# Kernel tuning notes

Measured on AMD Instinct MI355X. Metric: run time of the kernel, lower is better.

Reference implementation:

```python
import math
import jax, jax.numpy as jnp
import numpy as np

B, N, D, Pd, L, H = 2, 384, 256, 64, 8, 8
Dh = D // H
VOCAB = 21


def _layernorm(x, w, b, eps=1e-5):
    m = jnp.mean(x, axis=-1, keepdims=True)
    v = jnp.var(x, axis=-1, keepdims=True)
    return (x - m) * jax.lax.rsqrt(v + eps) * w + b


def _safe_norm(v):
    return jnp.sqrt(jnp.sum(v * v, axis=-1, keepdims=True) + 1e-8)


def _rot6d(r6):
    # Zhou et al. 6D rotation -> 3x3 via Gram-Schmidt (rows b1,b2,b3)
    a1, a2 = r6[..., :3], r6[..., 3:6]
    b1 = a1 / _safe_norm(a1)
    a2p = a2 - jnp.sum(b1 * a2, axis=-1, keepdims=True) * b1
    b2 = a2p / _safe_norm(a2p)
    b3 = jnp.cross(b1, b2)
    return jnp.stack([b1, b2, b3], axis=-2)  # [..., 3, 3]


def _pos_enc(n, d):
    pos = jnp.arange(n, dtype=jnp.float32)[:, None]
    div = jnp.exp(jnp.arange(0, d, 2, dtype=jnp.float32) * (-math.log(10000.0) / d))
    ang = pos * div  # [n, d/2]
    return jnp.zeros((n, d), jnp.float32).at[:, 0::2].set(jnp.sin(ang)).at[:, 1::2].set(jnp.cos(ang))


def _se3_frame_attention(Q, K, V, frames):
    # Frame-conditioned attention: dot-product scores biased by squared
    # distance between frame translations (IPA-style point bias).
    t = frames[..., :3, 3]                                   # [B,N,3]
    d2 = jnp.sum((t[:, :, None] - t[:, None, :]) ** 2, -1)   # [B,N,N]
    s = jnp.einsum('bihd,bjhd->bhij', Q, K) / math.sqrt(Dh) - d2[:, None]
    a = jax.nn.softmax(s, axis=-1)
    return jnp.einsum('bhij,bjhd->bihd', a, V)               # [B,N,H,Dh]


def _encode(tokens, tok_emb, emb_ln_w, emb_ln_b, Wq, Wk, Wv, Wo, bo,
            attn_ln_w, attn_ln_b, ff_ln_w, ff_ln_b, W1, b1, W2, b2,
            Wop, bop, relpos_emb, pair_ln_w, pair_ln_b, Wf1, bf1, Wf2, bf2):
    Bb, Nn = tokens.shape
    x = tok_emb[tokens] + _pos_enc(Nn, D)[None]
    x = _layernorm(x, emb_ln_w, emb_ln_b)
    frames = jnp.broadcast_to(jnp.eye(4, dtype=x.dtype), (Bb, Nn, 4, 4))
    pos = jnp.arange(Nn)
    rel = jnp.clip(pos[None, :] - pos[:, None], -64, 64) + 64  # rel[i,j]=pos[j]-pos[i]
    rel_e = relpos_emb[rel]                                    # [N,N,Pd]
    bot = jnp.broadcast_to(jnp.array([0.0, 0.0, 0.0, 1.0], x.dtype), (Bb, Nn, 1, 4))
    for l in range(L):
        # SE3 attention block (dropout = identity in eval)
        Q = (x @ Wq[l]).reshape(Bb, Nn, H, Dh)
        Kh = (x @ Wk[l]).reshape(Bb, Nn, H, Dh)
        Vh = (x @ Wv[l]).reshape(Bb, Nn, H, Dh)
        ao = _se3_frame_attention(Q, Kh, Vh, frames).reshape(Bb, Nn, D)
        x = _layernorm(x + ao @ Wo[l] + bo[l], attn_ln_w[l], attn_ln_b[l])
        # FFN (pre-LN inside the Sequential), residual add
        h = _layernorm(x, ff_ln_w[l], ff_ln_b[l])
        x = x + (jax.nn.gelu(h @ W1[l] + b1[l], approximate=False) @ W2[l] + b2[l])
        # Pair features
        proj = jax.nn.relu(x @ Wop + bop)                      # [B,N,Pd]
        pair = _layernorm(proj[:, :, None] + proj[:, None, :] + rel_e[None],
                          pair_ln_w, pair_ln_b)                # [B,N,N,Pd]
        # Frame head
        feat = jnp.concatenate([x, pair.mean(axis=2)], axis=-1)
        raw = jax.nn.silu(feat @ Wf1 + bf1) @ Wf2 + bf2        # [B,N,9]
        R = _rot6d(raw[..., :6])
        trans = raw[..., 6:]
        top = jnp.concatenate([R, trans[..., None]], axis=-1)  # [B,N,3,4]
        frames = jnp.concatenate([top, bot], axis=-2)          # [B,N,4,4]
    return frames, x


def setup_inputs() -> dict:
    key = jax.random.key(0)
    ks = iter(jax.random.split(key, 16))
    def w(shape, scale):
        return (jax.random.normal(next(ks), shape) * scale).astype(jnp.float32)
    return {
        'tokens': jax.random.randint(next(ks), (B, N), 0, VOCAB, dtype=jnp.int32),
        'tok_emb': w((VOCAB, D), 0.02),
        'emb_ln_w': jnp.ones((D,), jnp.float32), 'emb_ln_b': jnp.zeros((D,), jnp.float32),
        'Wq': w((L, D, D), D ** -0.5), 'Wk': w((L, D, D), D ** -0.5),
        'Wv': w((L, D, D), D ** -0.5), 'Wo': w((L, D, D), D ** -0.5),
        'bo': jnp.zeros((L, D), jnp.float32),
        'attn_ln_w': jnp.ones((L, D), jnp.float32), 'attn_ln_b': jnp.zeros((L, D), jnp.float32),
        'ff_ln_w': jnp.ones((L, D), jnp.float32), 'ff_ln_b': jnp.zeros((L, D), jnp.float32),
        'W1': w((L, D, 4 * D), D ** -0.5), 'b1': jnp.zeros((L, 4 * D), jnp.float32),
        'W2': w((L, 4 * D, D), (4 * D) ** -0.5), 'b2': jnp.zeros((L, D), jnp.float32),
        'Wop': w((D, Pd), D ** -0.5), 'bop': jnp.zeros((Pd,), jnp.float32),
        'relpos_emb': w((129, Pd), 0.02),
        'pair_ln_w': jnp.ones((Pd,), jnp.float32), 'pair_ln_b': jnp.zeros((Pd,), jnp.float32),
        'Wf1': w((D + Pd, 128), (D + Pd) ** -0.5), 'bf1': jnp.zeros((128,), jnp.float32),
        'Wf2': w((128, 9), 128 ** -0.5), 'bf2': jnp.zeros((9,), jnp.float32),
    }


def reference(tokens, tok_emb, emb_ln_w, emb_ln_b, Wq, Wk, Wv, Wo, bo,
              attn_ln_w, attn_ln_b, ff_ln_w, ff_ln_b, W1, b1, W2, b2,
              Wop, bop, relpos_emb, pair_ln_w, pair_ln_b, Wf1, bf1, Wf2, bf2):
    return _encode(tokens, tok_emb, emb_ln_w, emb_ln_b, Wq, Wk, Wv, Wo, bo,
                   attn_ln_w, attn_ln_b, ff_ln_w, ff_ln_b, W1, b1, W2, b2,
                   Wop, bop, relpos_emb, pair_ln_w, pair_ln_b, Wf1, bf1, Wf2, bf2)
```

## Files before the change

### kernel.cpp

```cpp
#include <hip/hip_runtime.h>
#include <hip/hip_bf16.h>
#include <math.h>

#define B_  2
#define N_  384
#define D_  256
#define PD_ 64
#define L_  8
#define H_  8
#define DH_ 32
#define GR  4
#define IT  8
#define RT_ 132

__global__ void prologue_kernel(const int* __restrict__ tokens, const float* __restrict__ tok_emb,
                                const float* __restrict__ lnw, const float* __restrict__ lnb,
                                const float* __restrict__ relpos,
                                float* __restrict__ x, float* __restrict__ frames,
                                float* __restrict__ tx, float* __restrict__ ty,
                                float* __restrict__ tz,
                                float* __restrict__ relc, float* __restrict__ relcT) {
  int row = blockIdx.x;
  int n = row % N_;
  int d = threadIdx.x;
  __shared__ float rbuf[256];
  __shared__ float smr;
  if (d < 16) frames[row * 16 + d] = (d == 0 || d == 5 || d == 10 || d == 15) ? 1.0f : 0.0f;
  if (d == 16) tx[row] = 0.0f;
  if (d == 17) ty[row] = 0.0f;
  if (d == 18) tz[row] = 0.0f;
  if (row < 129 && d >= 192) {
    int lane = d & 63;
    float s = relpos[row * PD_ + lane];
    #pragma unroll
    for (int off = 32; off >= 1; off >>= 1) s += __shfl_xor(s, off, 64);
    if (lane == 0) smr = s * (1.0f / PD_);
  }
  int tok = tokens[row];
  float val = tok_emb[tok * D_ + d];
  int i = d >> 1;
  float dv = expf((float)(2 * i) * (-logf(10000.0f) / (float)D_));
  float ang = (float)n * dv;
  val += (d & 1) ? cosf(ang) : sinf(ang);
  rbuf[d] = val; __syncthreads();
  for (int s = 128; s > 0; s >>= 1) { if (d < s) rbuf[d] += rbuf[d + s]; __syncthreads(); }
  float mean = rbuf[0] / D_;
  __syncthreads();
  rbuf[d] = val * val; __syncthreads();
  for (int s = 128; s > 0; s >>= 1) { if (d < s) rbuf[d] += rbuf[d + s]; __syncthreads(); }
  float var = rbuf[0] / D_ - mean * mean;
  float r = rsqrtf(var + 1e-5f);
  x[row * D_ + d] = (val - mean) * r * lnw[d] + lnb[d];
  if (row < 129 && d < PD_) {
    float cv = relpos[row * PD_ + d] - smr;
    relc[row * PD_ + d] = cv;
    relcT[d * RT_ + row] = cv;
  }
}

__device__ __forceinline__ void qkv_unit(int bid, int tid, const float* __restrict__ x,
                                         const float* __restrict__ Wq, const float* __restrict__ Wk,
                                         const float* __restrict__ Wv,
                                         float* __restrict__ q, float* __restrict__ kt,
                                         float* __restrict__ v, float* sA) {
  int tile = bid & 3;
  int m = (bid >> 2) % 3;
  int r0 = (bid / 12) * GR;
  float* red = sA + GR * D_;
  {
    int r = tid >> 6, lane = tid & 63;
    ((float4*)(sA + r * D_))[lane] = ((const float4*)(x + (size_t)(r0 + r) * D_))[lane];
  }
  __syncthreads();
  const float* W = (m == 0) ? Wq : (m == 1) ? Wk : Wv;
  int kc = tid >> 6, c = tid & 63;
  const float* wp = W + (size_t)(kc * 64) * D_ + tile * 64 + c;
  const float* s0 = sA + kc * 64;
  float a0 = 0.f, a1 = 0.f, a2 = 0.f, a3 = 0.f;
  for (int kk = 0; kk < 64; kk += 4) {
    float w0 = wp[(size_t)kk * D_], w1 = wp[(size_t)(kk + 1) * D_];
    float w2 = wp[(size_t)(kk + 2) * D_], w3 = wp[(size_t)(kk + 3) * D_];
    float4 h0 = *(const float4*)(s0 + 0 * D_ + kk);
    float4 h1 = *(const float4*)(s0 + 1 * D_ + kk);
    float4 h2 = *(const float4*)(s0 + 2 * D_ + kk);
    float4 h3 = *(const float4*)(s0 + 3 * D_ + kk);
    a0 = fmaf(h0.x, w0, fmaf(h0.y, w1, fmaf(h0.z, w2, fmaf(h0.w, w3, a0))));
    a1 = fmaf(h1.x, w0, fmaf(h1.y, w1, fmaf(h1.z, w2, fmaf(h1.w, w3, a1))));
    a2 = fmaf(h2.x, w0, fmaf(h2.y, w1, fmaf(h2.z, w2, fmaf(h2.w, w3, a2))));
    a3 = fmaf(h3.x, w0, fmaf(h3.y, w1, fmaf(h3.z, w2, fmaf(h3.w, w3, a3))));
  }
  red[(kc * 4 + 0) * 64 + c] = a0;
  red[(kc * 4 + 1) * 64 + c] = a1;
  red[(kc * 4 + 2) * 64 + c] = a2;
  red[(kc * 4 + 3) * 64 + c] = a3;
  __syncthreads();
  int r = tid >> 6;
  float s = red[(0 * 4 + r) * 64 + c] + red[(1 * 4 + r) * 64 + c]
          + red[(2 * 4 + r) * 64 + c] + red[(3 * 4 + r) * 64 + c];
  int col = tile * 64 + c;
  int row = r0 + r;
  if (m == 1) {
    int b = row / N_, j = row % N_;
    int hh = col >> 5, dd = col & 31;
    kt[((size_t)(b * H_ + hh) * DH_ + dd) * N_ + j] = s;
  } else {
    float* O = (m == 0) ? q : v;
    O[(size_t)row * D_ + col] = s;
  }
}

__device__ __forceinline__ void proj_unit(int row, int tid, const float* __restrict__ x,
                                          const float* __restrict__ Wop, const float* __restrict__ bop,
                                          float* __restrict__ projc, float* __restrict__ projcT,
                                          float* smem) {
  float* sA  = smem;
  float* red = smem + 256;
  if (tid < 64) ((float4*)sA)[tid] = ((const float4*)(x + (size_t)row * D_))[tid];
  __syncthreads();
  int kc = tid >> 6, c = tid & 63;
  const float* wp = Wop + (kc * 64) * PD_ + c;
  const float* s0 = sA + kc * 64;
  float a0 = 0.f, a1 = 0.f, a2 = 0.f, a3 = 0.f;
  for (int kk = 0; kk < 64; kk += 4) {
    a0 = fmaf(s0[kk],     wp[(kk)     * PD_], a0);
    a1 = fmaf(s0[kk + 1], wp[(kk + 1) * PD_], a1);
    a2 = fmaf(s0[kk + 2], wp[(kk + 2) * PD_], a2);
    a3 = fmaf(s0[kk + 3], wp[(kk + 3) * PD_], a3);
  }
  red[kc * 64 + c] = (a0 + a1) + (a2 + a3);
  __syncthreads();
  if (tid < 64) {
    float acc = fmaxf(bop[tid] + red[tid] + red[64 + tid] + red[128 + tid] + red[192 + tid], 0.0f);
    float s = acc;
    #pragma unroll
    for (int off = 32; off >= 1; off >>= 1) s += __shfl_xor(s, off, 64);
    float cv = acc - s * (1.0f / PD_);
    projc[row * PD_ + tid] = cv;
    projcT[(size_t)tid * (B_ * N_) + row] = cv;
  }
}

__global__ void qkv_kernel(const float* __restrict__ x, const float* __restrict__ Wq,
                           const float* __restrict__ Wk, const float* __restrict__ Wv,
                           float* __restrict__ q, float* __restrict__ kt, float* __restrict__ v) {
  __shared__ __align__(16) float smem[2048];
  qkv_unit(blockIdx.x, threadIdx.x, x, Wq, Wk, Wv, q, kt, v, smem);
}

__global__ void proj_qkv_kernel(const float* __restrict__ x,
                                const float* __restrict__ Wop, const float* __restrict__ bop,
                                float* __restrict__ projc, float* __restrict__ projcT,
                                const float* __restrict__ Wq, const float* __restrict__ Wk,
                                const float* __restrict__ Wv,
                                float* __restrict__ q, float* __restrict__ kt,
                                float* __restrict__ v) {
  __shared__ __align__(16) float smem[2048];
  int bid = blockIdx.x, tid = threadIdx.x;
  if (bid < B_ * N_) proj_unit(bid, tid, x, Wop, bop, projc, projcT, smem);
  else               qkv_unit(bid - B_ * N_, tid, x, Wq, Wk, Wv, q, kt, v, smem);
}

__global__ void wo_ln_kernel(const float* __restrict__ ao, const float* __restrict__ Wo,
                             const float* __restrict__ bo,
                             const float* __restrict__ lnw, const float* __restrict__ lnb,
                             float* xio, float* __restrict__ xout) {
  int r0 = blockIdx.x * 2;
  int tid = threadIdx.x;
  int wave = tid >> 6, lane = tid & 63;
  __shared__ __align__(16) float sAO[2 * D_];
  __shared__ float wred[4][4];
  if (tid < 128) ((float4*)sAO)[tid] = ((const float4*)(ao + (size_t)r0 * D_))[tid];
  __syncthreads();
  const float* wp = Wo + tid;
  float a0 = 0.f, a1 = 0.f, a2 = 0.f, a3 = 0.f;
  float c0 = 0.f, c1 = 0.f, c2 = 0.f, c3 = 0.f;
  for (int kk = 0; kk < D_; kk += 4) {
    float w0 = wp[(size_t)kk * D_], w1 = wp[(size_t)(kk + 1) * D_];
    float w2 = wp[(size_t)(kk + 2) * D_], w3 = wp[(size_t)(kk + 3) * D_];
    float4 h0 = *(const float4*)(sAO + kk);
    float4 h1 = *(const float4*)(sAO + D_ + kk);
    a0 = fmaf(h0.x, w0, a0); a1 = fmaf(h0.y, w1, a1);
    a2 = fmaf(h0.z, w2, a2); a3 = fmaf(h0.w, w3, a3);
    c0 = fmaf(h1.x, w0, c0); c1 = fmaf(h1.y, w1, c1);
    c2 = fmaf(h1.z, w2, c2); c3 = fmaf(h1.w, w3, c3);
  }
  float bb = bo[tid];
  float v0 = xio[(size_t)r0 * D_ + tid]       + bb + (a0 + a1) + (a2 + a3);
  float v1 = xio[(size_t)(r0 + 1) * D_ + tid] + bb + (c0 + c1) + (c2 + c3);
  float s0 = v0, q0 = v0 * v0, s1 = v1, q1 = v1 * v1;
  #pragma unroll
  for (int off = 32; off >= 1; off >>= 1) {
    s0 += __shfl_xor(s0, off, 64); q0 += __shfl_xor(q0, off, 64);
    s1 += __shfl_xor(s1, off, 64); q1 += __shfl_xor(q1, off, 64);
  }
  if (lane == 0) {
    wred[0][wave] = s0; wred[1][wave] = q0;
    wred[2][wave] = s1; wred[3][wave] = q1;
  }
  __syncthreads();
  float S0 = wred[0][0] + wred[0][1] + wred[0][2] + wred[0][3];
  float Q0 = wred[1][0] + wred[1][1] + wred[1][2] + wred[1][3];
  float S1 = wred[2][0] + wred[2][1] + wred[2][2] + wred[2][3];
  float Q1 = wred[3][0] + wred[3][1] + wred[3][2] + wred[3][3];
  float m0 = S0 * (1.0f / D_), m1 = S1 * (1.0f / D_);
  float r0v = rsqrtf(Q0 * (1.0f / D_) - m0 * m0 + 1e-5f);
  float r1v = rsqrtf(Q1 * (1.0f / D_) - m1 * m1 + 1e-5f);
  float wv = lnw[tid], bv = lnb[tid];
  xout[(size_t)r0 * D_ + tid]       = (v0 - m0) * r0v * wv + bv;
  xout[(size_t)(r0 + 1) * D_ + tid] = (v1 - m1) * r1v * wv + bv;
  xio[(size_t)r0 * D_ + tid]       = 0.0f;
  xio[(size_t)(r0 + 1) * D_ + tid] = 0.0f;
}

__global__ void ff_fused_kernel(const float* __restrict__ xs,
                                const float* __restrict__ lnw, const float* __restrict__ lnb,
                                const float* __restrict__ W1, const float* __restrict__ b1,
                                const float* __restrict__ W2, const float* __restrict__ b2v,
                                float* __restrict__ xacc) {
  int bid = blockIdx.x;
  int tile = bid & 7;
  int r0 = (bid >> 3) * GR;
  int tid = threadIdx.x;
  __shared__ __align__(16) float sA[GR * D_];
  __shared__ float red[2 * GR * 128];
  __shared__ __align__(16) float sF[128 * 4];
  {
    int r = tid >> 6, lane = tid & 63;
    float4 v = ((const float4*)(xs + (size_t)(r0 + r) * D_))[lane];
    float s = v.x + v.y + v.z + v.w;
    float s2 = v.x * v.x + v.y * v.y + v.z * v.z + v.w * v.w;
    #pragma unroll
    for (int off = 32; off >= 1; off >>= 1) {
      s  += __shfl_xor(s, off, 64);
      s2 += __shfl_xor(s2, off, 64);
    }
    float mean = s * (1.0f / D_);
    float var = s2 * (1.0f / D_) - mean * mean;
    float rin = rsqrtf(var + 1e-5f);
    float4 w4 = ((const float4*)lnw)[lane];
    float4 b4 = ((const float4*)lnb)[lane];
    float4 nv;
    nv.x = (v.x - mean) * rin * w4.x + b4.x;
    nv.y = (v.y - mean) * rin * w4.y + b4.y;
    nv.z = (v.z - mean) * rin * w4.z + b4.z;
    nv.w = (v.w - mean) * rin * w4.w + b4.w;
    ((float4*)(sA + r * D_))[lane] = nv;
  }
  __syncthreads();
  {
    int kc = tid >> 7, c = tid & 127;
    int col = tile * 128 + c;
    const float* wp = W1 + (size_t)(kc * 128) * 1024 + col;
    const float* s0 = sA + kc * 128;
    float a0 = 0.f, a1 = 0.f, a2 = 0.f, a3 = 0.f;
    for (int kk = 0; kk < 128; kk += 4) {
      float w0 = wp[(size_t)kk * 1024], w1 = wp[(size_t)(kk + 1) * 1024];
      float w2 = wp[(size_t)(kk + 2) * 1024], w3 = wp[(size_t)(kk + 3) * 1024];
      float4 h0 = *(const float4*)(s0 + 0 * D_ + kk);
      float4 h1 = *(const float4*)(s0 + 1 * D_ + kk);
      float4 h2 = *(const float4*)(s0 + 2 * D_ + kk);
      float4 h3 = *(const float4*)(s0 + 3 * D_ + kk);
      a0 = fmaf(h0.x, w0, fmaf(h0.y, w1, fmaf(h0.z, w2, fmaf(h0.w, w3, a0))));
      a1 = fmaf(h1.x, w0, fmaf(h1.y, w1, fmaf(h1.z, w2, fmaf(h1.w, w3, a1))));
      a2 = fmaf(h2.x, w0, fmaf(h2.y, w1, fmaf(h2.z, w2, fmaf(h2.w, w3, a2))));
      a3 = fmaf(h3.x, w0, fmaf(h3.y, w1, fmaf(h3.z, w2, fmaf(h3.w, w3, a3))));
    }
    red[(kc * 4 + 0) * 128 + c] = a0;
    red[(kc * 4 + 1) * 128 + c] = a1;
    red[(kc * 4 + 2) * 128 + c] = a2;
    red[(kc * 4 + 3) * 128 + c] = a3;
  }
  __syncthreads();
  {
    int rA = tid >> 7, c = tid & 127;
    int col = tile * 128 + c;
    #pragma unroll
    for (int p = 0; p < 2; p++) {
      int r = rA + p * 2;
      float s = red[(0 * 4 + r) * 128 + c] + red[(1 * 4 + r) * 128 + c] + b1[col];
      s = 0.5f * s * (1.0f + erff(s * 0.7071067811865475f));
      sF[c * 4 + r] = s;
    }
  }
  __syncthreads();
  {
    const float* w2p = W2 + (size_t)(tile * 128) * D_ + tid;
    float o0 = 0.f, o1 = 0.f, o2 = 0.f, o3 = 0.f;
    #pragma unroll 8
    for (int k = 0; k < 128; k++) {
      float w = w2p[(size_t)k * D_];
      float4 f4 = *(const float4*)(sF + k * 4);
      o0 = fmaf(f4.x, w, o0); o1 = fmaf(f4.y, w, o1);
      o2 = fmaf(f4.z, w, o2); o3 = fmaf(f4.w, w, o3);
    }
    if (tile == 0) {
      float bb2 = b2v[tid];
      o0 += xs[(size_t)(r0 + 0) * D_ + tid] + bb2;
      o1 += xs[(size_t)(r0 + 1) * D_ + tid] + bb2;
      o2 += xs[(size_t)(r0 + 2) * D_ + tid] + bb2;
      o3 += xs[(size_t)(r0 + 3) * D_ + tid] + bb2;
    }
    atomicAdd(&xacc[(size_t)(r0 + 0) * D_ + tid], o0);
    atomicAdd(&xacc[(size_t)(r0 + 1) * D_ + tid], o1);
    atomicAdd(&xacc[(size_t)(r0 + 2) * D_ + tid], o2);
    atomicAdd(&xacc[(size_t)(r0 + 3) * D_ + tid], o3);
  }
}

__global__ void attn_kernel(const float* __restrict__ Q, const float* __restrict__ KT,
                            const float* __restrict__ V,
                            const float* __restrict__ tx, const float* __restrict__ ty,
                            const float* __restrict__ tz, float* __restrict__ AO) {
  const int TILES = N_ / IT;
  int bid = blockIdx.x;
  int it = bid % TILES;
  int h  = (bid / TILES) % H_;
  int b  = bid / (TILES * H_);
  int i0 = it * IT;
  int tid = threadIdx.x;
  int wave = tid >> 6, lane = tid & 63;

  __shared__ __align__(16) float sQ[IT * DH_];
  __shared__ __align__(16) float sK[DH_ * 64];
  __shared__ __align__(16) float sV[64 * DH_];
  __shared__ __align__(16) float sS[IT][N_];
  __shared__ float sti[3][IT];
  __shared__ float sinv[IT];

  {
    int ii = tid >> 5, d = tid & 31;
    sQ[ii * DH_ + d] = Q[((size_t)(b * N_ + i0 + ii)) * D_ + h * DH_ + d];
  }
  if (tid < IT) {
    sti[0][tid] = tx[b * N_ + i0 + tid];
    sti[1][tid] = ty[b * N_ + i0 + tid];
    sti[2][tid] = tz[b * N_ + i0 + tid];
  }
  const float* ktb = KT + (size_t)(b * H_ + h) * DH_ * N_;
  const float* vb  = V + (size_t)b * N_ * D_ + h * DH_;
  const float* txb = tx + b * N_;
  const float* tyb = ty + b * N_;
  const float* tzb = tz + b * N_;
  __syncthreads();

  float4 q0r[8], q1r[8];
  #pragma unroll
  for (int t = 0; t < 8; t++) {
    q0r[t] = ((const float4*)(sQ + (wave * 2 + 0) * DH_))[t];
    q1r[t] = ((const float4*)(sQ + (wave * 2 + 1) * DH_))[t];
  }

  for (int jc = 0; jc < N_; jc += 64) {
    for (int idx = tid; idx < DH_ * 64; idx += 256) {
      int d = idx >> 6, jj = idx & 63;
      sK[d * 64 + jj] = ktb[(size_t)d * N_ + jc + jj];
    }
    __syncthreads();
    int jj = lane;
    float tjx = txb[jc + jj], tjy = tyb[jc + jj], tjz = tzb[jc + jj];
    float a0 = 0.f, a1 = 0.f;
    #pragma unroll
    for (int t = 0; t < 8; t++) {
      float k0 = sK[(4 * t + 0) * 64 + jj];
      float k1 = sK[(4 * t + 1) * 64 + jj];
      float k2 = sK[(4 * t + 2) * 64 + jj];
      float k3 = sK[(4 * t + 3) * 64 + jj];
      float4 qa = q0r[t], qb = q1r[t];
      a0 = fmaf(qa.x, k0, fmaf(qa.y, k1, fmaf(qa.z, k2, fmaf(qa.w, k3, a0))));
      a1 = fmaf(qb.x, k0, fmaf(qb.y, k1, fmaf(qb.z, k2, fmaf(qb.w, k3, a1))));
    }
    #pragma unroll
    for (int s = 0; s < 2; s++) {
      int ii = wave * 2 + s;
      float a = (s == 0) ? a0 : a1;
      float dx = sti[0][ii] - tjx;
      float dy = sti[1][ii] - tjy;
      float dz = sti[2][ii] - tjz;
      sS[ii][jc + jj] = a * 0.17677669529663689f - (dx * dx + dy * dy + dz * dz);
    }
    __syncthreads();
  }

  #pragma unroll
  for (int s = 0; s < 2; s++) {
    int ii = wave * 2 + s;
    float vrow[6];
    float m = -1e30f;
    #pragma unroll
    for (int t = 0; t < 6; t++) { vrow[t] = sS[ii][t * 64 + lane]; m = fmaxf(m, vrow[t]); }
    #pragma unroll
    for (int off = 32; off >= 1; off >>= 1) m = fmaxf(m, __shfl_xor(m, off, 64));
    float ps = 0.f;
    #pragma unroll
    for (int t = 0; t < 6; t++) {
      float e = expf(vrow[t] - m);
      sS[ii][t * 64 + lane] = e;
      ps += e;
    }
    #pragma unroll
    for (int off = 32; off >= 1; off >>= 1) ps += __shfl_xor(ps, off, 64);
    if (lane == 0) sinv[ii] = 1.0f / ps;
  }
  __syncthreads();

  int ii = tid >> 5, dd = tid & 31;
  float o0 = 0.f, o1 = 0.f;
  for (int jc = 0; jc < N_; jc += 64) {
    for (int idx = tid; idx < 64 * DH_; idx += 256) {
      int jj = idx >> 5, d = idx & 31;
      sV[jj * DH_ + d] = vb[(size_t)(jc + jj) * D_ + d];
    }
    __syncthreads();
    const float* srow = &sS[ii][jc];
    #pragma unroll
    for (int jj = 0; jj < 64; jj += 4) {
      float4 sv = *(const float4*)(srow + jj);
      o0 = fmaf(sv.x, sV[(jj + 0) * DH_ + dd], o0);
      o1 = fmaf(sv.y, sV[(jj + 1) * DH_ + dd], o1);
      o0 = fmaf(sv.z, sV[(jj + 2) * DH_ + dd], o0);
      o1 = fmaf(sv.w, sV[(jj + 3) * DH_ + dd], o1);
    }
    __syncthreads();
  }
  AO[((size_t)(b * N_ + i0 + ii)) * D_ + h * DH_ + dd] = (o0 + o1) * sinv[ii];
}

__global__ void pair_head_kernel(const float* __restrict__ projc, const float* __restrict__ projcT,
                                 const float* __restrict__ relc, const float* __restrict__ relcT,
                                 const float* __restrict__ lnw, const float* __restrict__ lnb,
                                 const float* __restrict__ x,
                                 const float* __restrict__ Wf1, const float* __restrict__ bWf1,
                                 const float* __restrict__ Wf2, const float* __restrict__ bWf2,
                                 float* __restrict__ frames, float* __restrict__ tx,
                                 float* __restrict__ ty, float* __restrict__ tz) {
  const int M = B_ * N_;
  int row = blockIdx.x;
  int b = row / N_;
  int i = row % N_;
  int tid = threadIdx.x;
  int lane = tid & 63;
  int wave = tid >> 6;
  __shared__ float svpi[PD_];
  __shared__ float sr[N_];
  __shared__ float red[4][PD_];
  __shared__ float sfeat[320];
  __shared__ float fred[2][128];
  __shared__ float sg[128];
  __shared__ float sraw[9];

  if (tid < PD_) svpi[tid] = projc[row * PD_ + tid];
  if (tid < D_) sfeat[tid] = x[(size_t)row * D_ + tid];
  __syncthreads();

  {
    int jA = tid;
    int raA = jA - i; raA = raA < -64 ? -64 : (raA > 64 ? 64 : raA); raA += 64;
    const float* pA = projcT + b * N_ + jA;
    const float* rA = relcT + raA;
    float s2A = 0.f;
    #pragma unroll 8
    for (int c = 0; c < PD_; c++) {
      float dA = svpi[c] + pA[(size_t)c * M] + rA[c * RT_];
      s2A = fmaf(dA, dA, s2A);
    }
    sr[jA] = rsqrtf(s2A * (1.0f / PD_) + 1e-5f);
    if (tid < 128) {
      int jB = tid + 256;
      int raB = jB - i; raB = raB < -64 ? -64 : (raB > 64 ? 64 : raB); raB += 64;
      const float* pB = projcT + b * N_ + jB;
      const float* rB = relcT + raB;
      float s2B = 0.f;
      #pragma unroll 8
      for (int c = 0; c < PD_; c++) {
        float dB = svpi[c] + pB[(size_t)c * M] + rB[c * RT_];
        s2B = fmaf(dB, dB, s2B);
      }
      sr[jB] = rsqrtf(s2B * (1.0f / PD_) + 1e-5f);
    }
  }
  __syncthreads();

  {
    float vpl = svpi[lane];
    const float* pb = projc + (size_t)b * N_ * PD_;
    float acc = 0.0f;
    for (int j = wave * 2; j < N_; j += 8) {
      int ja = j, jb = j + 1;
      int ra = ja - i; ra = ra < -64 ? -64 : (ra > 64 ? 64 : ra); ra += 64;
      int rb = jb - i; rb = rb < -64 ? -64 : (rb > 64 ? 64 : rb); rb += 64;
      float da = vpl + pb[ja * PD_ + lane] + relc[ra * PD_ + lane];
      float db = vpl + pb[jb * PD_ + lane] + relc[rb * PD_ + lane];
      acc = fmaf(da, sr[ja], fmaf(db, sr[jb], acc));
    }
    red[wave][lane] = acc;
  }
  __syncthreads();
  if (wave == 0) {
    float s = red[0][lane] + red[1][lane] + red[2][lane] + red[3][lane];
    sfeat[D_ + lane] = lnb[lane] + s * lnw[lane] * (1.0f / N_);
  }
  __syncthreads();

  int kc = tid >> 7, c = tid & 127;
  int koff = kc * 160;
  const float* wp = Wf1 + (size_t)koff * 128 + c;
  const float* s0 = sfeat + koff;
  float a0 = 0.f, a1 = 0.f, a2 = 0.f, a3 = 0.f;
  for (int kk = 0; kk < 160; kk += 4) {
    a0 = fmaf(s0[kk],     wp[(size_t)kk * 128],       a0);
    a1 = fmaf(s0[kk + 1], wp[(size_t)(kk + 1) * 128], a1);
    a2 = fmaf(s0[kk + 2], wp[(size_t)(kk + 2) * 128], a2);
    a3 = fmaf(s0[kk + 3], wp[(size_t)(kk + 3) * 128], a3);
  }
  fred[kc][c] = (a0 + a1) + (a2 + a3);
  __syncthreads();
  if (tid < 128) {
    float g = fred[0][tid] + fred[1][tid] + bWf1[tid];
    sg[tid] = g / (1.0f + expf(-g));
  }
  __syncthreads();

  if (tid < 9) {
    float b0 = 0.f, b1v = 0.f;
    for (int kk = 0; kk < 128; kk += 2) {
      b0  = fmaf(sg[kk],     Wf2[(kk)     * 9 + tid], b0);
      b1v = fmaf(sg[kk + 1], Wf2[(kk + 1) * 9 + tid], b1v);
    }
    sraw[tid] = bWf2[tid] + b0 + b1v;
  }
  __syncthreads();
  if (tid == 0) {
    float a1x = sraw[0], a1y = sraw[1], a1z = sraw[2];
    float a2x = sraw[3], a2y = sraw[4], a2z = sraw[5];
    float n1 = sqrtf(a1x * a1x + a1y * a1y + a1z * a1z + 1e-8f);
    float b1x = a1x / n1, b1y = a1y / n1, b1z = a1z / n1;
    float dp = b1x * a2x + b1y * a2y + b1z * a2z;
    float px = a2x - dp * b1x, py = a2y - dp * b1y, pz = a2z - dp * b1z;
    float n2 = sqrtf(px * px + py * py + pz * pz + 1e-8f);
    float b2x = px / n2, b2y = py / n2, b2z = pz / n2;
    float b3x = b1y * b2z - b1z * b2y;
    float b3y = b1z * b2x - b1x * b2z;
    float b3z = b1x * b2y - b1y * b2x;
    float* f = frames + row * 16;
    f[0]  = b1x; f[1]  = b1y; f[2]  = b1z; f[3]  = sraw[6];
    f[4]  = b2x; f[5]  = b2y; f[6]  = b2z; f[7]  = sraw[7];
    f[8]  = b3x; f[9]  = b3y; f[10] = b3z; f[11] = sraw[8];
    f[12] = 0.0f; f[13] = 0.0f; f[14] = 0.0f; f[15] = 1.0f;
    tx[row] = sraw[6];
    ty[row] = sraw[7];
    tz[row] = sraw[8];
  }
}

__global__ void write_out_kernel(const float* __restrict__ frames, const float* __restrict__ x,
                                 float* __restrict__ out) {
  int i = blockIdx.x * 256 + threadIdx.x;
  const int nf = B_ * N_ * 16;
  const int total = nf + B_ * N_ * D_;
  if (i < nf) out[i] = frames[i];
  else if (i < total) out[i] = x[i - nf];
}

extern "C" void kernel_launch(void* const* d_in, const int* in_sizes, int n_in,
                              void* d_out, int out_size, void* d_ws, size_t ws_size,
                              hipStream_t stream) {
  const int*   tokens    = (const int*)  d_in[0];
  const float* tok_emb   = (const float*)d_in[1];
  const float* emb_ln_w  = (const float*)d_in[2];
  const float* emb_ln_b  = (const float*)d_in[3];
  const float* Wq        = (const float*)d_in[4];
  const float* Wk        = (const float*)d_in[5];
  const float* Wv        = (const float*)d_in[6];
  const float* Wo        = (const float*)d_in[7];
  const float* bo        = (const float*)d_in[8];
  const float* attn_ln_w = (const float*)d_in[9];
  const float* attn_ln_b = (const float*)d_in[10];
  const float* ff_ln_w   = (const float*)d_in[11];
  const float* ff_ln_b   = (const float*)d_in[12];
  const float* W1        = (const float*)d_in[13];
  const float* b1        = (const float*)d_in[14];
  const float* W2        = (const float*)d_in[15];
  const float* b2        = (const float*)d_in[16];
  const float* Wop       = (const float*)d_in[17];
  const float* bop       = (const float*)d_in[18];
  const float* relpos    = (const float*)d_in[19];
  const float* pair_ln_w = (const float*)d_in[20];
  const float* pair_ln_b = (const float*)d_in[21];
  const float* Wf1       = (const float*)d_in[22];
  const float* bWf1      = (const float*)d_in[23];
  const float* Wf2       = (const float*)d_in[24];
  const float* bWf2      = (const float*)d_in[25];

  const int M = B_ * N_;
  const int XE = M * D_;
  float* ws     = (float*)d_ws;
  float* frames = ws;
  float* projc  = frames + M * 16;
  float* projcT = projc  + M * PD_;
  float* relc   = projcT + M * PD_;
  float* relcT  = relc   + 8320;
  float* tx     = relcT  + 8448;
  float* ty     = tx     + M;
  float* tz     = ty     + M;
  float* xb     = tz     + M;
  float* q      = xb + XE;
  float* kt     = q  + XE;
  float* v      = kt + XE;
  float* ao     = v  + XE;
  float* xa     = ao + XE;

  prologue_kernel<<<M, 256, 0, stream>>>(tokens, tok_emb, emb_ln_w, emb_ln_b, relpos,
                                         xb, frames, tx, ty, tz, relc, relcT);
  qkv_kernel<<<(M / GR) * 12, 256, 0, stream>>>(xb, Wq, Wk, Wv, q, kt, v);

  for (int l = 0; l < L_; l++) {
    attn_kernel<<<B_ * H_ * (N_ / IT), 256, 0, stream>>>(q, kt, v, tx, ty, tz, ao);
    wo_ln_kernel<<<M / 2, 256, 0, stream>>>(ao, Wo + (size_t)l * D_ * D_, bo + l * D_,
                                            attn_ln_w + l * D_, attn_ln_b + l * D_, xb, xa);
    ff_fused_kernel<<<(M / GR) * 8, 256, 0, stream>>>(
        xa, ff_ln_w + l * D_, ff_ln_b + l * D_,
        W1 + (size_t)l * D_ * 1024, b1 + l * 1024,
        W2 + (size_t)l * 1024 * D_, b2 + l * D_, xb);
    if (l < L_ - 1) {
      int lq = l + 1;
      proj_qkv_kernel<<<M + (M / GR) * 12, 256, 0, stream>>>(
          xb, Wop, bop, projc, projcT,
          Wq + (size_t)lq * D_ * D_, Wk + (size_t)lq * D_ * D_, Wv + (size_t)lq * D_ * D_,
          q, kt, v);
    } else {
      proj_qkv_kernel<<<M, 256, 0, stream>>>(xb, Wop, bop, projc, projcT, Wq, Wk, Wv, q, kt, v);
    }
    pair_head_kernel<<<M, 256, 0, stream>>>(projc, projcT, relc, relcT, pair_ln_w, pair_ln_b,
                                            xb, Wf1, bWf1, Wf2, bWf2, frames, tx, ty, tz);
  }

  const int total = B_ * N_ * 16 + B_ * N_ * D_;
  write_out_kernel<<<(total + 255) / 256, 256, 0, stream>>>(frames, xb, (float*)d_out);
}
```

Measured before the change: 920.7 us.

## Fuse Wo projection into attention epilogue and merge attention LayerNorm into FF kernel

Each attention block now multiplies its head output by its slice of Wo and atomically adds the result directly into the residual buffer, so the separate wo_ln kernel and the ao buffer go away. The FF kernel adds the Wo bias, applies the attention LayerNorm and then the FF LayerNorm in one pass. It accumulates into a second ping-pong buffer that earlier kernels zero. This saves one launch per layer and a round trip of the attention output through global memory. In exchange it adds atomic contention across the 8 heads and extra zeroing stores.

```diff
diff --git a/kernel.cpp b/kernel.cpp
--- a/kernel.cpp
+++ b/kernel.cpp
@@ -19,7 +19,8 @@
                                 float* __restrict__ x, float* __restrict__ frames,
                                 float* __restrict__ tx, float* __restrict__ ty,
                                 float* __restrict__ tz,
-                                float* __restrict__ relc, float* __restrict__ relcT) {
+                                float* __restrict__ relc, float* __restrict__ relcT,
+                                float* __restrict__ xz) {
   int row = blockIdx.x;
   int n = row % N_;
   int d = threadIdx.x;
@@ -29,6 +30,7 @@
   if (d == 16) tx[row] = 0.0f;
   if (d == 17) ty[row] = 0.0f;
   if (d == 18) tz[row] = 0.0f;
+  xz[(size_t)row * D_ + d] = 0.0f;
   if (row < 129 && d >= 192) {
     int lane = d & 63;
     float s = relpos[row * PD_ + lane];
@@ -112,9 +114,10 @@
 __device__ __forceinline__ void proj_unit(int row, int tid, const float* __restrict__ x,
                                           const float* __restrict__ Wop, const float* __restrict__ bop,
                                           float* __restrict__ projc, float* __restrict__ projcT,
-                                          float* smem) {
+                                          float* __restrict__ zbuf, float* smem) {
   float* sA  = smem;
   float* red = smem + 256;
+  zbuf[(size_t)row * D_ + tid] = 0.0f;
   if (tid < 64) ((float4*)sA)[tid] = ((const float4*)(x + (size_t)row * D_))[tid];
   __syncthreads();
   int kc = tid >> 6, c = tid & 63;
@@ -153,80 +156,32 @@
                                 const float* __restrict__ Wq, const float* __restrict__ Wk,
                                 const float* __restrict__ Wv,
                                 float* __restrict__ q, float* __restrict__ kt,
-                                float* __restrict__ v) {
+                                float* __restrict__ v, float* __restrict__ zbuf) {
   __shared__ __align__(16) float smem[2048];
   int bid = blockIdx.x, tid = threadIdx.x;
-  if (bid < B_ * N_) proj_unit(bid, tid, x, Wop, bop, projc, projcT, smem);
+  if (bid < B_ * N_) proj_unit(bid, tid, x, Wop, bop, projc, projcT, zbuf, smem);
   else               qkv_unit(bid - B_ * N_, tid, x, Wq, Wk, Wv, q, kt, v, smem);
 }
 
-__global__ void wo_ln_kernel(const float* __restrict__ ao, const float* __restrict__ Wo,
-                             const float* __restrict__ bo,
-                             const float* __restrict__ lnw, const float* __restrict__ lnb,
-                             float* xio, float* __restrict__ xout) {
-  int r0 = blockIdx.x * 2;
-  int tid = threadIdx.x;
-  int wave = tid >> 6, lane = tid & 63;
-  __shared__ __align__(16) float sAO[2 * D_];
-  __shared__ float wred[4][4];
-  if (tid < 128) ((float4*)sAO)[tid] = ((const float4*)(ao + (size_t)r0 * D_))[tid];
-  __syncthreads();
-  const float* wp = Wo + tid;
-  float a0 = 0.f, a1 = 0.f, a2 = 0.f, a3 = 0.f;
-  float c0 = 0.f, c1 = 0.f, c2 = 0.f, c3 = 0.f;
-  for (int kk = 0; kk < D_; kk += 4) {
-    float w0 = wp[(size_t)kk * D_], w1 = wp[(size_t)(kk + 1) * D_];
-    float w2 = wp[(size_t)(kk + 2) * D_], w3 = wp[(size_t)(kk + 3) * D_];
-    float4 h0 = *(const float4*)(sAO + kk);
-    float4 h1 = *(const float4*)(sAO + D_ + kk);
-    a0 = fmaf(h0.x, w0, a0); a1 = fmaf(h0.y, w1, a1);
-    a2 = fmaf(h0.z, w2, a2); a3 = fmaf(h0.w, w3, a3);
-    c0 = fmaf(h1.x, w0, c0); c1 = fmaf(h1.y, w1, c1);
-    c2 = fmaf(h1.z, w2, c2); c3 = fmaf(h1.w, w3, c3);
-  }
-  float bb = bo[tid];
-  float v0 = xio[(size_t)r0 * D_ + tid]       + bb + (a0 + a1) + (a2 + a3);
-  float v1 = xio[(size_t)(r0 + 1) * D_ + tid] + bb + (c0 + c1) + (c2 + c3);
-  float s0 = v0, q0 = v0 * v0, s1 = v1, q1 = v1 * v1;
-  #pragma unroll
-  for (int off = 32; off >= 1; off >>= 1) {
-    s0 += __shfl_xor(s0, off, 64); q0 += __shfl_xor(q0, off, 64);
-    s1 += __shfl_xor(s1, off, 64); q1 += __shfl_xor(q1, off, 64);
-  }
-  if (lane == 0) {
-    wred[0][wave] = s0; wred[1][wave] = q0;
-    wred[2][wave] = s1; wred[3][wave] = q1;
-  }
-  __syncthreads();
-  float S0 = wred[0][0] + wred[0][1] + wred[0][2] + wred[0][3];
-  float Q0 = wred[1][0] + wred[1][1] + wred[1][2] + wred[1][3];
-  float S1 = wred[2][0] + wred[2][1] + wred[2][2] + wred[2][3];
-  float Q1 = wred[3][0] + wred[3][1] + wred[3][2] + wred[3][3];
-  float m0 = S0 * (1.0f / D_), m1 = S1 * (1.0f / D_);
-  float r0v = rsqrtf(Q0 * (1.0f / D_) - m0 * m0 + 1e-5f);
-  float r1v = rsqrtf(Q1 * (1.0f / D_) - m1 * m1 + 1e-5f);
-  float wv = lnw[tid], bv = lnb[tid];
-  xout[(size_t)r0 * D_ + tid]       = (v0 - m0) * r0v * wv + bv;
-  xout[(size_t)(r0 + 1) * D_ + tid] = (v1 - m1) * r1v * wv + bv;
-  xio[(size_t)r0 * D_ + tid]       = 0.0f;
-  xio[(size_t)(r0 + 1) * D_ + tid] = 0.0f;
-}
-
-__global__ void ff_fused_kernel(const float* __restrict__ xs,
-                                const float* __restrict__ lnw, const float* __restrict__ lnb,
+__global__ void ff_fused_kernel(const float* __restrict__ S, const float* __restrict__ bo,
+                                const float* __restrict__ alnw, const float* __restrict__ alnb,
+                                const float* __restrict__ flnw, const float* __restrict__ flnb,
                                 const float* __restrict__ W1, const float* __restrict__ b1,
                                 const float* __restrict__ W2, const float* __restrict__ b2v,
-                                float* __restrict__ xacc) {
+                                float* __restrict__ T) {
   int bid = blockIdx.x;
   int tile = bid & 7;
   int r0 = (bid >> 3) * GR;
   int tid = threadIdx.x;
   __shared__ __align__(16) float sA[GR * D_];
+  __shared__ __align__(16) float sX[GR * D_];
   __shared__ float red[2 * GR * 128];
   __shared__ __align__(16) float sF[128 * 4];
   {
     int r = tid >> 6, lane = tid & 63;
-    float4 v = ((const float4*)(xs + (size_t)(r0 + r) * D_))[lane];
+    float4 v = ((const float4*)(S + (size_t)(r0 + r) * D_))[lane];
+    float4 bo4 = ((const float4*)bo)[lane];
+    v.x += bo4.x; v.y += bo4.y; v.z += bo4.z; v.w += bo4.w;
     float s = v.x + v.y + v.z + v.w;
     float s2 = v.x * v.x + v.y * v.y + v.z * v.z + v.w * v.w;
     #pragma unroll
@@ -237,14 +192,32 @@
     float mean = s * (1.0f / D_);
     float var = s2 * (1.0f / D_) - mean * mean;
     float rin = rsqrtf(var + 1e-5f);
-    float4 w4 = ((const float4*)lnw)[lane];
-    float4 b4 = ((const float4*)lnb)[lane];
-    float4 nv;
-    nv.x = (v.x - mean) * rin * w4.x + b4.x;
-    nv.y = (v.y - mean) * rin * w4.y + b4.y;
-    nv.z = (v.z - mean) * rin * w4.z + b4.z;
-    nv.w = (v.w - mean) * rin * w4.w + b4.w;
-    ((float4*)(sA + r * D_))[lane] = nv;
+    float4 aw = ((const float4*)alnw)[lane];
+    float4 ab = ((const float4*)alnb)[lane];
+    float4 x4;
+    x4.x = (v.x - mean) * rin * aw.x + ab.x;
+    x4.y = (v.y - mean) * rin * aw.y + ab.y;
+    x4.z = (v.z - mean) * rin * aw.z + ab.z;
+    x4.w = (v.w - mean) * rin * aw.w + ab.w;
+    ((float4*)(sX + r * D_))[lane] = x4;
+    float t = x4.x + x4.y + x4.z + x4.w;
+    float t2 = x4.x * x4.x + x4.y * x4.y + x4.z * x4.z + x4.w * x4.w;
+    #pragma unroll
+    for (int off = 32; off >= 1; off >>= 1) {
+      t  += __shfl_xor(t, off, 64);
+      t2 += __shfl_xor(t2, off, 64);
+    }
+    float mean2 = t * (1.0f / D_);
+    float var2 = t2 * (1.0f / D_) - mean2 * mean2;
+    float rin2 = rsqrtf(var2 + 1e-5f);
+    float4 fw = ((const float4*)flnw)[lane];
+    float4 fb = ((const float4*)flnb)[lane];
+    float4 h4;
+    h4.x = (x4.x - mean2) * rin2 * fw.x + fb.x;
+    h4.y = (x4.y - mean2) * rin2 * fw.y + fb.y;
+    h4.z = (x4.z - mean2) * rin2 * fw.z + fb.z;
+    h4.w = (x4.w - mean2) * rin2 * fw.w + fb.w;
+    ((float4*)(sA + r * D_))[lane] = h4;
   }
   __syncthreads();
   {
@@ -295,22 +268,23 @@
     }
     if (tile == 0) {
       float bb2 = b2v[tid];
-      o0 += xs[(size_t)(r0 + 0) * D_ + tid] + bb2;
-      o1 += xs[(size_t)(r0 + 1) * D_ + tid] + bb2;
-      o2 += xs[(size_t)(r0 + 2) * D_ + tid] + bb2;
-      o3 += xs[(size_t)(r0 + 3) * D_ + tid] + bb2;
-    }
-    atomicAdd(&xacc[(size_t)(r0 + 0) * D_ + tid], o0);
-    atomicAdd(&xacc[(size_t)(r0 + 1) * D_ + tid], o1);
-    atomicAdd(&xacc[(size_t)(r0 + 2) * D_ + tid], o2);
-    atomicAdd(&xacc[(size_t)(r0 + 3) * D_ + tid], o3);
+      o0 += sX[0 * D_ + tid] + bb2;
+      o1 += sX[1 * D_ + tid] + bb2;
+      o2 += sX[2 * D_ + tid] + bb2;
+      o3 += sX[3 * D_ + tid] + bb2;
+    }
+    atomicAdd(&T[(size_t)(r0 + 0) * D_ + tid], o0);
+    atomicAdd(&T[(size_t)(r0 + 1) * D_ + tid], o1);
+    atomicAdd(&T[(size_t)(r0 + 2) * D_ + tid], o2);
+    atomicAdd(&T[(size_t)(r0 + 3) * D_ + tid], o3);
   }
 }
 
 __global__ void attn_kernel(const float* __restrict__ Q, const float* __restrict__ KT,
                             const float* __restrict__ V,
                             const float* __restrict__ tx, const float* __restrict__ ty,
-                            const float* __restrict__ tz, float* __restrict__ AO) {
+                            const float* __restrict__ tz,
+                            const float* __restrict__ Wo, float* __restrict__ S) {
   const int TILES = N_ / IT;
   int bid = blockIdx.x;
   int it = bid % TILES;
@@ -422,7 +396,29 @@
     }
     __syncthreads();
   }
-  AO[((size_t)(b * N_ + i0 + ii)) * D_ + h * DH_ + dd] = (o0 + o1) * sinv[ii];
+
+  sQ[tid] = (o0 + o1) * sinv[ii];
+  __syncthreads();
+  {
+    const float* wo = Wo + (size_t)(h * DH_) * D_ + tid;
+    float acc[8];
+    #pragma unroll
+    for (int r = 0; r < 8; r++) acc[r] = 0.f;
+    for (int k = 0; k < DH_; k += 4) {
+      float w0 = wo[(size_t)(k + 0) * D_];
+      float w1 = wo[(size_t)(k + 1) * D_];
+      float w2 = wo[(size_t)(k + 2) * D_];
+      float w3 = wo[(size_t)(k + 3) * D_];
+      #pragma unroll
+      for (int r = 0; r < 8; r++) {
+        float4 a4 = *(const float4*)(sQ + r * DH_ + k);
+        acc[r] = fmaf(a4.x, w0, fmaf(a4.y, w1, fmaf(a4.z, w2, fmaf(a4.w, w3, acc[r]))));
+      }
+    }
+    float* Sb = S + ((size_t)(b * N_ + i0)) * D_ + tid;
+    #pragma unroll
+    for (int r = 0; r < 8; r++) atomicAdd(Sb + (size_t)r * D_, acc[r]);
+  }
 }
 
 __global__ void pair_head_kernel(const float* __restrict__ projc, const float* __restrict__ projcT,
@@ -602,38 +598,41 @@
   float* tx     = relcT  + 8448;
   float* ty     = tx     + M;
   float* tz     = ty     + M;
-  float* xb     = tz     + M;
-  float* q      = xb + XE;
+  float* xA     = tz     + M;
+  float* xB     = xA + XE;
+  float* q      = xB + XE;
   float* kt     = q  + XE;
   float* v      = kt + XE;
-  float* ao     = v  + XE;
-  float* xa     = ao + XE;
 
   prologue_kernel<<<M, 256, 0, stream>>>(tokens, tok_emb, emb_ln_w, emb_ln_b, relpos,
-                                         xb, frames, tx, ty, tz, relc, relcT);
-  qkv_kernel<<<(M / GR) * 12, 256, 0, stream>>>(xb, Wq, Wk, Wv, q, kt, v);
+                                         xA, frames, tx, ty, tz, relc, relcT, xB);
+  qkv_kernel<<<(M / GR) * 12, 256, 0, stream>>>(xA, Wq, Wk, Wv, q, kt, v);
 
   for (int l = 0; l < L_; l++) {
-    attn_kernel<<<B_ * H_ * (N_ / IT), 256, 0, stream>>>(q, kt, v, tx, ty, tz, ao);
-    wo_ln_kernel<<<M / 2, 256, 0, stream>>>(ao, Wo + (size_t)l * D_ * D_, bo + l * D_,
-                                            attn_ln_w + l * D_, attn_ln_b + l * D_, xb, xa);
+    float* Sin  = (l & 1) ? xB : xA;
+    float* Sout = (l & 1) ? xA : xB;
+    attn_kernel<<<B_ * H_ * (N_ / IT), 256, 0, stream>>>(
+        q, kt, v, tx, ty, tz, Wo + (size_t)l * D_ * D_, Sin);
     ff_fused_kernel<<<(M / GR) * 8, 256, 0, stream>>>(
-        xa, ff_ln_w + l * D_, ff_ln_b + l * D_,
+        Sin, bo + l * D_,
+        attn_ln_w + l * D_, attn_ln_b + l * D_,
+        ff_ln_w + l * D_, ff_ln_b + l * D_,
         W1 + (size_t)l * D_ * 1024, b1 + l * 1024,
-        W2 + (size_t)l * 1024 * D_, b2 + l * D_, xb);
+        W2 + (size_t)l * 1024 * D_, b2 + l * D_, Sout);
     if (l < L_ - 1) {
       int lq = l + 1;
       proj_qkv_kernel<<<M + (M / GR) * 12, 256, 0, stream>>>(
-          xb, Wop, bop, projc, projcT,
+          Sout, Wop, bop, projc, projcT,
           Wq + (size_t)lq * D_ * D_, Wk + (size_t)lq * D_ * D_, Wv + (size_t)lq * D_ * D_,
-          q, kt, v);
+          q, kt, v, Sin);
     } else {
-      proj_qkv_kernel<<<M, 256, 0, stream>>>(xb, Wop, bop, projc, projcT, Wq, Wk, Wv, q, kt, v);
+      proj_qkv_kernel<<<M, 256, 0, stream>>>(Sout, Wop, bop, projc, projcT,
+                                             Wq, Wk, Wv, q, kt, v, Sin);
     }
     pair_head_kernel<<<M, 256, 0, stream>>>(projc, projcT, relc, relcT, pair_ln_w, pair_ln_b,
-                                            xb, Wf1, bWf1, Wf2, bWf2, frames, tx, ty, tz);
+                                            Sout, Wf1, bWf1, Wf2, bWf2, frames, tx, ty, tz);
   }
 
   const int total = B_ * N_ * 16 + B_ * N_ * D_;
-  write_out_kernel<<<(total + 255) / 256, 256, 0, stream>>>(frames, xb, (float*)d_out);
-}
+  write_out_kernel<<<(total + 255) / 256, 256, 0, stream>>>(frames, xA, (float*)d_out);
+}
```

After: 873.4 us. 5.1% less time.
